# Performance work log

Hardware: AMD Instinct MI355X
Metric: run time of the kernel (lower is better)

The kernel has to match this reference:

```python
import jax, jax.numpy as jnp
import numpy as np

N_NODES = 200000
D = 256
HID = 512
OUT = 2
NUM_GRAPHS = 512


def setup_inputs() -> dict:
    key = jax.random.key(0)
    ks = jax.random.split(key, 8)
    x = jax.random.normal(ks[0], (N_NODES, D), dtype=jnp.float32)
    batch = jnp.sort(jax.random.randint(ks[1], (N_NODES,), 0, NUM_GRAPHS, dtype=jnp.int32))
    # MLP params (Linear stores weight as [out, in] in torch; we use [in, out])
    W1 = jax.random.normal(ks[2], (D, HID), dtype=jnp.float32) / np.sqrt(D)
    b1 = jnp.zeros((HID,), dtype=jnp.float32)
    W2 = jax.random.normal(ks[3], (HID, HID), dtype=jnp.float32) / np.sqrt(HID)
    b2 = jnp.zeros((HID,), dtype=jnp.float32)
    W3 = jax.random.normal(ks[4], (HID, OUT), dtype=jnp.float32) / np.sqrt(HID)
    b3 = jnp.zeros((OUT,), dtype=jnp.float32)
    return {"final_node_embeddings": x, "batch_vector": batch,
            "W1": W1, "b1": b1, "W2": W2, "b2": b2, "W3": W3, "b3": b3}


def reference(final_node_embeddings, batch_vector, W1, b1, W2, b2, W3, b3):
    x = final_node_embeddings
    # segment max pooling over graphs; empty graphs -> zeros (matches original)
    seg = jax.ops.segment_max(x, batch_vector, num_segments=NUM_GRAPHS)  # [G, D]
    counts = jax.ops.segment_sum(jnp.ones((x.shape[0],), dtype=x.dtype),
                                 batch_vector, num_segments=NUM_GRAPHS)  # [G]
    g = jnp.where(counts[:, None] > 0, seg, jnp.zeros((), dtype=x.dtype))
    # readout MLP (dropout inactive at inference)
    h = jax.nn.relu(g @ W1 + b1)
    h = jax.nn.relu(h @ W2 + b2)
    return h @ W3 + b3
```

## Files before the change

### kernel.cpp

```cpp
#include <hip/hip_runtime.h>
#include <float.h>

#define N_NODES 200000
#define D 256
#define HID 512
#define OUTD 2
#define NG 512

__device__ __forceinline__ float4 fmax4(float4 a, float4 b) {
    return make_float4(fmaxf(a.x, b.x), fmaxf(a.y, b.y), fmaxf(a.z, b.z), fmaxf(a.w, b.w));
}
__device__ __forceinline__ float4 shflx4(float4 v, int mask) {
    return make_float4(__shfl_xor(v.x, mask), __shfl_xor(v.y, mask),
                       __shfl_xor(v.z, mask), __shfl_xor(v.w, mask));
}

__global__ void k_bounds(const int* __restrict__ batch, int* __restrict__ row_start, int n) {
    int i = blockIdx.x * blockDim.x + threadIdx.x;
    if (i >= n) return;
    int b  = batch[i];
    int bp = (i == 0) ? -1 : batch[i - 1];
    for (int g = bp + 1; g <= b; ++g) row_start[g] = i;
    if (i == n - 1) {
        for (int g = b + 1; g <= NG; ++g) row_start[g] = n;
    }
}

__global__ __launch_bounds__(256) void k_pool(const float* __restrict__ x,
                                              const int* __restrict__ rs,
                                              float* __restrict__ gp) {
    const int g    = blockIdx.x;
    const int t    = threadIdx.x;
    const int lane = t & 63;
    const int wave = t >> 6;
    const int r0 = rs[g];
    const int r1 = rs[g + 1];
    const int len = r1 - r0;

    const float4 NEUT = make_float4(-FLT_MAX, -FLT_MAX, -FLT_MAX, -FLT_MAX);
    float4 m0 = NEUT, m1 = NEUT, m2 = NEUT, m3 = NEUT;

    if (len > 0) {
        const int rlast = r1 - 1;
        const int sub = lane >> 4;
        const int cq  = (lane & 15) * 16;
        const int iters = (len + 15) >> 4;
        for (int i = 0; i < iters; ++i) {
            int row = r0 + i * 16 + wave * 4 + sub;
            row = min(row, rlast);
            const float* p = x + (size_t)row * D + cq;
            float4 v0 = *reinterpret_cast<const float4*>(p);
            float4 v1 = *reinterpret_cast<const float4*>(p + 4);
            float4 v2 = *reinterpret_cast<const float4*>(p + 8);
            float4 v3 = *reinterpret_cast<const float4*>(p + 12);
            m0 = fmax4(m0, v0); m1 = fmax4(m1, v1);
            m2 = fmax4(m2, v2); m3 = fmax4(m3, v3);
        }
    }

    m0 = fmax4(m0, shflx4(m0, 16)); m0 = fmax4(m0, shflx4(m0, 32));
    m1 = fmax4(m1, shflx4(m1, 16)); m1 = fmax4(m1, shflx4(m1, 32));
    m2 = fmax4(m2, shflx4(m2, 16)); m2 = fmax4(m2, shflx4(m2, 32));
    m3 = fmax4(m3, shflx4(m3, 16)); m3 = fmax4(m3, shflx4(m3, 32));

    __shared__ float red[4][16][16];
    if (lane < 16) {
        *reinterpret_cast<float4*>(&red[wave][lane][0])  = m0;
        *reinterpret_cast<float4*>(&red[wave][lane][4])  = m1;
        *reinterpret_cast<float4*>(&red[wave][lane][8])  = m2;
        *reinterpret_cast<float4*>(&red[wave][lane][12]) = m3;
    }
    __syncthreads();
    {
        const int cg = t >> 4, e = t & 15;
        float o = fmaxf(fmaxf(red[0][cg][e], red[1][cg][e]),
                        fmaxf(red[2][cg][e], red[3][cg][e]));
        gp[(size_t)g * D + t] = (len > 0) ? o : 0.f;
    }
}

template <int K, bool RELU>
__global__ __launch_bounds__(256) void k_gemm(const float* __restrict__ A,
                                              const float* __restrict__ B,
                                              const float* __restrict__ bias,
                                              float* __restrict__ C, int N) {
    __shared__ float As[32][33];
    __shared__ float Bs[32][33];
    const int t  = threadIdx.x;
    const int bm = blockIdx.y * 32;
    const int bn = blockIdx.x * 32;
    const int lr = t >> 3;
    const int lc = (t & 7) << 2;
    const int tx = t & 15;
    const int ty = t >> 4;
    float acc00 = 0.f, acc01 = 0.f, acc10 = 0.f, acc11 = 0.f;

    for (int k0 = 0; k0 < K; k0 += 32) {
        float4 av = *reinterpret_cast<const float4*>(A + (size_t)(bm + lr) * K + k0 + lc);
        float4 bv = *reinterpret_cast<const float4*>(B + (size_t)(k0 + lr) * N + bn + lc);
        __syncthreads();
        As[lr][lc] = av.x; As[lr][lc + 1] = av.y; As[lr][lc + 2] = av.z; As[lr][lc + 3] = av.w;
        Bs[lr][lc] = bv.x; Bs[lr][lc + 1] = bv.y; Bs[lr][lc + 2] = bv.z; Bs[lr][lc + 3] = bv.w;
        __syncthreads();
#pragma unroll
        for (int kk = 0; kk < 32; ++kk) {
            float a0 = As[ty * 2][kk], a1 = As[ty * 2 + 1][kk];
            float b0 = Bs[kk][tx * 2], b1 = Bs[kk][tx * 2 + 1];
            acc00 += a0 * b0; acc01 += a0 * b1;
            acc10 += a1 * b0; acc11 += a1 * b1;
        }
    }

    const int r = bm + ty * 2, c = bn + tx * 2;
    float bc0 = bias[c], bc1 = bias[c + 1];
    float v00 = acc00 + bc0, v01 = acc01 + bc1;
    float v10 = acc10 + bc0, v11 = acc11 + bc1;
    if (RELU) {
        v00 = fmaxf(v00, 0.f); v01 = fmaxf(v01, 0.f);
        v10 = fmaxf(v10, 0.f); v11 = fmaxf(v11, 0.f);
    }
    C[(size_t)r * N + c]           = v00;
    C[(size_t)r * N + c + 1]       = v01;
    C[(size_t)(r + 1) * N + c]     = v10;
    C[(size_t)(r + 1) * N + c + 1] = v11;
}

__global__ __launch_bounds__(256) void k_fc3(const float* __restrict__ h,
                                             const float* __restrict__ W,
                                             const float* __restrict__ b,
                                             float* __restrict__ out) {
    const int wave = threadIdx.x >> 6;
    const int lane = threadIdx.x & 63;
    const int e = blockIdx.x * 4 + wave;
    const int row = e >> 1, col = e & 1;
    float s = 0.f;
#pragma unroll
    for (int k = lane; k < HID; k += 64)
        s += h[(size_t)row * HID + k] * W[(size_t)k * OUTD + col];
#pragma unroll
    for (int off = 32; off; off >>= 1) s += __shfl_xor(s, off);
    if (lane == 0) out[e] = s + b[col];
}

extern "C" void kernel_launch(void* const* d_in, const int* in_sizes, int n_in,
                              void* d_out, int out_size, void* d_ws, size_t ws_size,
                              hipStream_t stream) {
    const float* x     = (const float*)d_in[0];
    const int*   batch = (const int*)d_in[1];
    const float* W1    = (const float*)d_in[2];
    const float* b1    = (const float*)d_in[3];
    const float* W2    = (const float*)d_in[4];
    const float* b2    = (const float*)d_in[5];
    const float* W3    = (const float*)d_in[6];
    const float* b3    = (const float*)d_in[7];
    float* out = (float*)d_out;

    char* ws = (char*)d_ws;
    int*   row_start = (int*)ws;
    float* gp = (float*)(ws + 4096);
    float* h1 = (float*)(ws + 4096 + 512 * 1024);
    float* h2 = (float*)(ws + 4096 + 512 * 1024 + 1024 * 1024);

    k_bounds<<<(N_NODES + 255) / 256, 256, 0, stream>>>(batch, row_start, N_NODES);
    k_pool<<<NG, 256, 0, stream>>>(x, row_start, gp);
    k_gemm<D,   true ><<<dim3(HID / 32, NG / 32), 256, 0, stream>>>(gp, W1, b1, h1, HID);
    k_gemm<HID, true ><<<dim3(HID / 32, NG / 32), 256, 0, stream>>>(h1, W2, b2, h2, HID);
    k_fc3<<<NG * OUTD / 4, 256, 0, stream>>>(h2, W3, b3, out);
}
```

Measured before the change: 67.43 us.

## Fuse segment-max pooling and the full readout MLP into one per-graph kernel

Replaces the pool kernel, the two tiled GEMM kernels and the final FC kernel with a single kernel that runs one block per graph. Each block pools its rows into shared memory and then computes the three MLP layers as shared-memory GEMVs. This removes three launches and the global round-trips for the pooled vectors and hidden activations. In exchange, every block re-reads all of W1 and W2 (about 1.5MB), which means hundreds of MB of weight traffic served from cache instead of a reused tiled GEMM.

```diff
diff --git a/kernel.cpp b/kernel.cpp
--- a/kernel.cpp
+++ b/kernel.cpp
@@ -26,13 +26,26 @@
     }
 }
 
-__global__ __launch_bounds__(256) void k_pool(const float* __restrict__ x,
-                                              const int* __restrict__ rs,
-                                              float* __restrict__ gp) {
+__global__ __launch_bounds__(256) void k_fused(const float* __restrict__ x,
+                                               const int* __restrict__ rs,
+                                               const float* __restrict__ W1,
+                                               const float* __restrict__ b1,
+                                               const float* __restrict__ W2,
+                                               const float* __restrict__ b2,
+                                               const float* __restrict__ W3,
+                                               const float* __restrict__ b3,
+                                               float* __restrict__ out) {
     const int g    = blockIdx.x;
     const int t    = threadIdx.x;
     const int lane = t & 63;
     const int wave = t >> 6;
+
+    __shared__ float gr[D];
+    __shared__ float h1s[HID];
+    __shared__ float h2s[HID];
+    __shared__ float red[4][16][16];
+    __shared__ float fin[4][2];
+
     const int r0 = rs[g];
     const int r1 = rs[g + 1];
     const int len = r1 - r0;
@@ -63,7 +76,6 @@
     m2 = fmax4(m2, shflx4(m2, 16)); m2 = fmax4(m2, shflx4(m2, 32));
     m3 = fmax4(m3, shflx4(m3, 16)); m3 = fmax4(m3, shflx4(m3, 32));
 
-    __shared__ float red[4][16][16];
     if (lane < 16) {
         *reinterpret_cast<float4*>(&red[wave][lane][0])  = m0;
         *reinterpret_cast<float4*>(&red[wave][lane][4])  = m1;
@@ -75,71 +87,65 @@
         const int cg = t >> 4, e = t & 15;
         float o = fmaxf(fmaxf(red[0][cg][e], red[1][cg][e]),
                         fmaxf(red[2][cg][e], red[3][cg][e]));
-        gp[(size_t)g * D + t] = (len > 0) ? o : 0.f;
+        gr[t] = (len > 0) ? o : 0.f;
     }
-}
+    __syncthreads();
 
-template <int K, bool RELU>
-__global__ __launch_bounds__(256) void k_gemm(const float* __restrict__ A,
-                                              const float* __restrict__ B,
-                                              const float* __restrict__ bias,
-                                              float* __restrict__ C, int N) {
-    __shared__ float As[32][33];
-    __shared__ float Bs[32][33];
-    const int t  = threadIdx.x;
-    const int bm = blockIdx.y * 32;
-    const int bn = blockIdx.x * 32;
-    const int lr = t >> 3;
-    const int lc = (t & 7) << 2;
-    const int tx = t & 15;
-    const int ty = t >> 4;
-    float acc00 = 0.f, acc01 = 0.f, acc10 = 0.f, acc11 = 0.f;
+    {
+        float a0 = 0.f, a1 = 0.f;
+        const float* w = W1 + 2 * t;
+#pragma unroll 4
+        for (int k = 0; k < D; k += 4) {
+            float4 xa = *reinterpret_cast<const float4*>(&gr[k]);
+            float2 w0 = *reinterpret_cast<const float2*>(w + (size_t)(k)     * HID);
+            float2 w1 = *reinterpret_cast<const float2*>(w + (size_t)(k + 1) * HID);
+            float2 w2 = *reinterpret_cast<const float2*>(w + (size_t)(k + 2) * HID);
+            float2 w3 = *reinterpret_cast<const float2*>(w + (size_t)(k + 3) * HID);
+            a0 += xa.x * w0.x + xa.y * w1.x + xa.z * w2.x + xa.w * w3.x;
+            a1 += xa.x * w0.y + xa.y * w1.y + xa.z * w2.y + xa.w * w3.y;
+        }
+        float2 bb = *reinterpret_cast<const float2*>(b1 + 2 * t);
+        h1s[2 * t]     = fmaxf(a0 + bb.x, 0.f);
+        h1s[2 * t + 1] = fmaxf(a1 + bb.y, 0.f);
+    }
+    __syncthreads();
 
-    for (int k0 = 0; k0 < K; k0 += 32) {
-        float4 av = *reinterpret_cast<const float4*>(A + (size_t)(bm + lr) * K + k0 + lc);
-        float4 bv = *reinterpret_cast<const float4*>(B + (size_t)(k0 + lr) * N + bn + lc);
+    {
+        float a0 = 0.f, a1 = 0.f;
+        const float* w = W2 + 2 * t;
+#pragma unroll 4
+        for (int k = 0; k < HID; k += 4) {
+            float4 xa = *reinterpret_cast<const float4*>(&h1s[k]);
+            float2 w0 = *reinterpret_cast<const float2*>(w + (size_t)(k)     * HID);
+            float2 w1 = *reinterpret_cast<const float2*>(w + (size_t)(k + 1) * HID);
+            float2 w2 = *reinterpret_cast<const float2*>(w + (size_t)(k + 2) * HID);
+            float2 w3 = *reinterpret_cast<const float2*>(w + (size_t)(k + 3) * HID);
+            a0 += xa.x * w0.x + xa.y * w1.x + xa.z * w2.x + xa.w * w3.x;
+            a1 += xa.x * w0.y + xa.y * w1.y + xa.z * w2.y + xa.w * w3.y;
+        }
+        float2 bb = *reinterpret_cast<const float2*>(b2 + 2 * t);
+        h2s[2 * t]     = fmaxf(a0 + bb.x, 0.f);
+        h2s[2 * t + 1] = fmaxf(a1 + bb.y, 0.f);
+    }
+    __syncthreads();
+
+    {
+        float4 w = *reinterpret_cast<const float4*>(W3 + 4 * t);
+        float2 h = *reinterpret_cast<const float2*>(&h2s[2 * t]);
+        float p0 = h.x * w.x + h.y * w.z;
+        float p1 = h.x * w.y + h.y * w.w;
+#pragma unroll
+        for (int off = 32; off; off >>= 1) {
+            p0 += __shfl_xor(p0, off);
+            p1 += __shfl_xor(p1, off);
+        }
+        if (lane == 0) { fin[wave][0] = p0; fin[wave][1] = p1; }
         __syncthreads();
-        As[lr][lc] = av.x; As[lr][lc + 1] = av.y; As[lr][lc + 2] = av.z; As[lr][lc + 3] = av.w;
-        Bs[lr][lc] = bv.x; Bs[lr][lc + 1] = bv.y; Bs[lr][lc + 2] = bv.z; Bs[lr][lc + 3] = bv.w;
-        __syncthreads();
-#pragma unroll
-        for (int kk = 0; kk < 32; ++kk) {
-            float a0 = As[ty * 2][kk], a1 = As[ty * 2 + 1][kk];
-            float b0 = Bs[kk][tx * 2], b1 = Bs[kk][tx * 2 + 1];
-            acc00 += a0 * b0; acc01 += a0 * b1;
-            acc10 += a1 * b0; acc11 += a1 * b1;
+        if (t < 2) {
+            float s = fin[0][t] + fin[1][t] + fin[2][t] + fin[3][t];
+            out[(size_t)g * OUTD + t] = s + b3[t];
         }
     }
-
-    const int r = bm + ty * 2, c = bn + tx * 2;
-    float bc0 = bias[c], bc1 = bias[c + 1];
-    float v00 = acc00 + bc0, v01 = acc01 + bc1;
-    float v10 = acc10 + bc0, v11 = acc11 + bc1;
-    if (RELU) {
-        v00 = fmaxf(v00, 0.f); v01 = fmaxf(v01, 0.f);
-        v10 = fmaxf(v10, 0.f); v11 = fmaxf(v11, 0.f);
-    }
-    C[(size_t)r * N + c]           = v00;
-    C[(size_t)r * N + c + 1]       = v01;
-    C[(size_t)(r + 1) * N + c]     = v10;
-    C[(size_t)(r + 1) * N + c + 1] = v11;
-}
-
-__global__ __launch_bounds__(256) void k_fc3(const float* __restrict__ h,
-                                             const float* __restrict__ W,
-                                             const float* __restrict__ b,
-                                             float* __restrict__ out) {
-    const int wave = threadIdx.x >> 6;
-    const int lane = threadIdx.x & 63;
-    const int e = blockIdx.x * 4 + wave;
-    const int row = e >> 1, col = e & 1;
-    float s = 0.f;
-#pragma unroll
-    for (int k = lane; k < HID; k += 64)
-        s += h[(size_t)row * HID + k] * W[(size_t)k * OUTD + col];
-#pragma unroll
-    for (int off = 32; off; off >>= 1) s += __shfl_xor(s, off);
-    if (lane == 0) out[e] = s + b[col];
 }
 
 extern "C" void kernel_launch(void* const* d_in, const int* in_sizes, int n_in,
@@ -155,15 +161,8 @@
     const float* b3    = (const float*)d_in[7];
     float* out = (float*)d_out;
 
-    char* ws = (char*)d_ws;
-    int*   row_start = (int*)ws;
-    float* gp = (float*)(ws + 4096);
-    float* h1 = (float*)(ws + 4096 + 512 * 1024);
-    float* h2 = (float*)(ws + 4096 + 512 * 1024 + 1024 * 1024);
+    int* row_start = (int*)d_ws;
 
     k_bounds<<<(N_NODES + 255) / 256, 256, 0, stream>>>(batch, row_start, N_NODES);
-    k_pool<<<NG, 256, 0, stream>>>(x, row_start, gp);
-    k_gemm<D,   true ><<<dim3(HID / 32, NG / 32), 256, 0, stream>>>(gp, W1, b1, h1, HID);
-    k_gemm<HID, true ><<<dim3(HID / 32, NG / 32), 256, 0, stream>>>(h1, W2, b2, h2, HID);
-    k_fc3<<<NG * OUTD / 4, 256, 0, stream>>>(h2, W3, b3, out);
+    k_fused<<<NG, 256, 0, stream>>>(x, row_start, W1, b1, W2, b2, W3, b3, out);
 }
```

Result: slower. 82.31 us (+22.1%).

## Split segment-max pooling into four row slices per graph and merge in GEMM1

Applied to the files above, without the earlier changes.

Each graph's rows are split across four blocks instead of one, giving 2048 pooling blocks instead of 512 to better fill the GPU for the memory-bound 200MB read. Each thread also loads two rows per iteration into independent accumulators for more memory-level parallelism. The four partial maxima are combined, with the empty-graph zero check, while loading the A tile in the first GEMM. This adds a 2MB scratch buffer and extra reads in GEMM1.

```diff
diff --git a/kernel.cpp b/kernel.cpp
--- a/kernel.cpp
+++ b/kernel.cpp
@@ -6,6 +6,7 @@
 #define HID 512
 #define OUTD 2
 #define NG 512
+#define SLICES 4
 
 __device__ __forceinline__ float4 fmax4(float4 a, float4 b) {
     return make_float4(fmaxf(a.x, b.x), fmaxf(a.y, b.y), fmaxf(a.z, b.z), fmaxf(a.w, b.w));
@@ -28,35 +29,54 @@
 
 __global__ __launch_bounds__(256) void k_pool(const float* __restrict__ x,
                                               const int* __restrict__ rs,
-                                              float* __restrict__ gp) {
-    const int g    = blockIdx.x;
+                                              float* __restrict__ scr) {
+    const int blk  = blockIdx.x;
+    const int g    = blk >> 2;
+    const int q    = blk & 3;
     const int t    = threadIdx.x;
     const int lane = t & 63;
     const int wave = t >> 6;
-    const int r0 = rs[g];
-    const int r1 = rs[g + 1];
-    const int len = r1 - r0;
+
+    const int r0g = rs[g];
+    const int r1g = rs[g + 1];
+    const int len = r1g - r0g;
+    const int c   = (len + SLICES - 1) >> 2;
+    const int s0  = r0g + q * c;
+    const int s1  = min(s0 + c, r1g);
+    const int slen = s1 - s0;
 
     const float4 NEUT = make_float4(-FLT_MAX, -FLT_MAX, -FLT_MAX, -FLT_MAX);
-    float4 m0 = NEUT, m1 = NEUT, m2 = NEUT, m3 = NEUT;
-
-    if (len > 0) {
-        const int rlast = r1 - 1;
+    float4 mA0 = NEUT, mA1 = NEUT, mA2 = NEUT, mA3 = NEUT;
+    float4 mB0 = NEUT, mB1 = NEUT, mB2 = NEUT, mB3 = NEUT;
+
+    if (slen > 0) {
+        const int rlast = s1 - 1;
         const int sub = lane >> 4;
         const int cq  = (lane & 15) * 16;
-        const int iters = (len + 15) >> 4;
+        const int iters = (slen + 31) >> 5;
         for (int i = 0; i < iters; ++i) {
-            int row = r0 + i * 16 + wave * 4 + sub;
-            row = min(row, rlast);
-            const float* p = x + (size_t)row * D + cq;
-            float4 v0 = *reinterpret_cast<const float4*>(p);
-            float4 v1 = *reinterpret_cast<const float4*>(p + 4);
-            float4 v2 = *reinterpret_cast<const float4*>(p + 8);
-            float4 v3 = *reinterpret_cast<const float4*>(p + 12);
-            m0 = fmax4(m0, v0); m1 = fmax4(m1, v1);
-            m2 = fmax4(m2, v2); m3 = fmax4(m3, v3);
+            int rowA = s0 + i * 32 + wave * 4 + sub;
+            int rowB = rowA + 16;
+            rowA = min(rowA, rlast);
+            rowB = min(rowB, rlast);
+            const float* pA = x + (size_t)rowA * D + cq;
+            const float* pB = x + (size_t)rowB * D + cq;
+            float4 a0 = *reinterpret_cast<const float4*>(pA);
+            float4 a1 = *reinterpret_cast<const float4*>(pA + 4);
+            float4 a2 = *reinterpret_cast<const float4*>(pA + 8);
+            float4 a3 = *reinterpret_cast<const float4*>(pA + 12);
+            float4 b0 = *reinterpret_cast<const float4*>(pB);
+            float4 b1 = *reinterpret_cast<const float4*>(pB + 4);
+            float4 b2 = *reinterpret_cast<const float4*>(pB + 8);
+            float4 b3 = *reinterpret_cast<const float4*>(pB + 12);
+            mA0 = fmax4(mA0, a0); mA1 = fmax4(mA1, a1);
+            mA2 = fmax4(mA2, a2); mA3 = fmax4(mA3, a3);
+            mB0 = fmax4(mB0, b0); mB1 = fmax4(mB1, b1);
+            mB2 = fmax4(mB2, b2); mB3 = fmax4(mB3, b3);
         }
     }
+    float4 m0 = fmax4(mA0, mB0), m1 = fmax4(mA1, mB1);
+    float4 m2 = fmax4(mA2, mB2), m3 = fmax4(mA3, mB3);
 
     m0 = fmax4(m0, shflx4(m0, 16)); m0 = fmax4(m0, shflx4(m0, 32));
     m1 = fmax4(m1, shflx4(m1, 16)); m1 = fmax4(m1, shflx4(m1, 32));
@@ -75,15 +95,66 @@
         const int cg = t >> 4, e = t & 15;
         float o = fmaxf(fmaxf(red[0][cg][e], red[1][cg][e]),
                         fmaxf(red[2][cg][e], red[3][cg][e]));
-        gp[(size_t)g * D + t] = (len > 0) ? o : 0.f;
-    }
-}
-
-template <int K, bool RELU>
-__global__ __launch_bounds__(256) void k_gemm(const float* __restrict__ A,
-                                              const float* __restrict__ B,
-                                              const float* __restrict__ bias,
-                                              float* __restrict__ C, int N) {
+        scr[(size_t)blk * D + t] = o;
+    }
+}
+
+__global__ __launch_bounds__(256) void k_gemm1(const float* __restrict__ scr,
+                                               const int* __restrict__ rs,
+                                               const float* __restrict__ B,
+                                               const float* __restrict__ bias,
+                                               float* __restrict__ C, int N) {
+    __shared__ float As[32][33];
+    __shared__ float Bs[32][33];
+    const int t  = threadIdx.x;
+    const int bm = blockIdx.y * 32;
+    const int bn = blockIdx.x * 32;
+    const int lr = t >> 3;
+    const int lc = (t & 7) << 2;
+    const int tx = t & 15;
+    const int ty = t >> 4;
+
+    const int grow = bm + lr;
+    const bool nonempty = rs[grow + 1] > rs[grow];
+    const float* srow = scr + (size_t)grow * 4 * D;
+
+    float acc00 = 0.f, acc01 = 0.f, acc10 = 0.f, acc11 = 0.f;
+
+    for (int k0 = 0; k0 < D; k0 += 32) {
+        float4 a0 = *reinterpret_cast<const float4*>(srow + 0 * D + k0 + lc);
+        float4 a1 = *reinterpret_cast<const float4*>(srow + 1 * D + k0 + lc);
+        float4 a2 = *reinterpret_cast<const float4*>(srow + 2 * D + k0 + lc);
+        float4 a3 = *reinterpret_cast<const float4*>(srow + 3 * D + k0 + lc);
+        float4 av = fmax4(fmax4(a0, a1), fmax4(a2, a3));
+        if (!nonempty) av = make_float4(0.f, 0.f, 0.f, 0.f);
+        float4 bv = *reinterpret_cast<const float4*>(B + (size_t)(k0 + lr) * N + bn + lc);
+        __syncthreads();
+        As[lr][lc] = av.x; As[lr][lc + 1] = av.y; As[lr][lc + 2] = av.z; As[lr][lc + 3] = av.w;
+        Bs[lr][lc] = bv.x; Bs[lr][lc + 1] = bv.y; Bs[lr][lc + 2] = bv.z; Bs[lr][lc + 3] = bv.w;
+        __syncthreads();
+#pragma unroll
+        for (int kk = 0; kk < 32; ++kk) {
+            float a0s = As[ty * 2][kk], a1s = As[ty * 2 + 1][kk];
+            float b0s = Bs[kk][tx * 2], b1s = Bs[kk][tx * 2 + 1];
+            acc00 += a0s * b0s; acc01 += a0s * b1s;
+            acc10 += a1s * b0s; acc11 += a1s * b1s;
+        }
+    }
+
+    const int r = bm + ty * 2, cc = bn + tx * 2;
+    float bc0 = bias[cc], bc1 = bias[cc + 1];
+    float v00 = fmaxf(acc00 + bc0, 0.f), v01 = fmaxf(acc01 + bc1, 0.f);
+    float v10 = fmaxf(acc10 + bc0, 0.f), v11 = fmaxf(acc11 + bc1, 0.f);
+    C[(size_t)r * N + cc]           = v00;
+    C[(size_t)r * N + cc + 1]       = v01;
+    C[(size_t)(r + 1) * N + cc]     = v10;
+    C[(size_t)(r + 1) * N + cc + 1] = v11;
+}
+
+__global__ __launch_bounds__(256) void k_gemm2(const float* __restrict__ A,
+                                               const float* __restrict__ B,
+                                               const float* __restrict__ bias,
+                                               float* __restrict__ C, int N) {
     __shared__ float As[32][33];
     __shared__ float Bs[32][33];
     const int t  = threadIdx.x;
@@ -95,8 +166,8 @@
     const int ty = t >> 4;
     float acc00 = 0.f, acc01 = 0.f, acc10 = 0.f, acc11 = 0.f;
 
-    for (int k0 = 0; k0 < K; k0 += 32) {
-        float4 av = *reinterpret_cast<const float4*>(A + (size_t)(bm + lr) * K + k0 + lc);
+    for (int k0 = 0; k0 < HID; k0 += 32) {
+        float4 av = *reinterpret_cast<const float4*>(A + (size_t)(bm + lr) * HID + k0 + lc);
         float4 bv = *reinterpret_cast<const float4*>(B + (size_t)(k0 + lr) * N + bn + lc);
         __syncthreads();
         As[lr][lc] = av.x; As[lr][lc + 1] = av.y; As[lr][lc + 2] = av.z; As[lr][lc + 3] = av.w;
@@ -113,12 +184,8 @@
 
     const int r = bm + ty * 2, c = bn + tx * 2;
     float bc0 = bias[c], bc1 = bias[c + 1];
-    float v00 = acc00 + bc0, v01 = acc01 + bc1;
-    float v10 = acc10 + bc0, v11 = acc11 + bc1;
-    if (RELU) {
-        v00 = fmaxf(v00, 0.f); v01 = fmaxf(v01, 0.f);
-        v10 = fmaxf(v10, 0.f); v11 = fmaxf(v11, 0.f);
-    }
+    float v00 = fmaxf(acc00 + bc0, 0.f), v01 = fmaxf(acc01 + bc1, 0.f);
+    float v10 = fmaxf(acc10 + bc0, 0.f), v11 = fmaxf(acc11 + bc1, 0.f);
     C[(size_t)r * N + c]           = v00;
     C[(size_t)r * N + c + 1]       = v01;
     C[(size_t)(r + 1) * N + c]     = v10;
@@ -157,13 +224,13 @@
 
     char* ws = (char*)d_ws;
     int*   row_start = (int*)ws;
-    float* gp = (float*)(ws + 4096);
-    float* h1 = (float*)(ws + 4096 + 512 * 1024);
-    float* h2 = (float*)(ws + 4096 + 512 * 1024 + 1024 * 1024);
+    float* scr = (float*)(ws + 4096);
+    float* h1  = (float*)(ws + 4096 + 2 * 1024 * 1024);
+    float* h2  = (float*)(ws + 4096 + 3 * 1024 * 1024);
 
     k_bounds<<<(N_NODES + 255) / 256, 256, 0, stream>>>(batch, row_start, N_NODES);
-    k_pool<<<NG, 256, 0, stream>>>(x, row_start, gp);
-    k_gemm<D,   true ><<<dim3(HID / 32, NG / 32), 256, 0, stream>>>(gp, W1, b1, h1, HID);
-    k_gemm<HID, true ><<<dim3(HID / 32, NG / 32), 256, 0, stream>>>(h1, W2, b2, h2, HID);
+    k_pool<<<NG * SLICES, 256, 0, stream>>>(x, row_start, scr);
+    k_gemm1<<<dim3(HID / 32, NG / 32), 256, 0, stream>>>(scr, row_start, W1, b1, h1, HID);
+    k_gemm2<<<dim3(HID / 32, NG / 32), 256, 0, stream>>>(h1, W2, b2, h2, HID);
     k_fc3<<<NG * OUTD / 4, 256, 0, stream>>>(h2, W3, b3, out);
 }
```

Result: slower. 70.47 us (+4.5%).
